# Kernel tuning notes

Measured on AMD Instinct MI355X. Metric: run time of the kernel, lower is better.

Reference implementation:

```python
import jax, jax.numpy as jnp
import numpy as np

N_NODES = 102400
N_EDGES = 1638400
NUM_GRAPHS = 128
IN_DIM = 128
HID = 128
OUT_DIM = 2
NUM_LAYERS = 3
BN_EPS = 1e-5


def setup_inputs() -> dict:
    key = jax.random.key(0)
    ks = jax.random.split(key, 12)
    x = jax.random.normal(ks[0], (N_NODES, IN_DIM), dtype=jnp.float32)
    edge_index = jax.random.randint(ks[1], (2, N_EDGES), 0, N_NODES, dtype=jnp.int64)
    # 128 graphs of 800 nodes each, sorted segment ids
    batch = jnp.repeat(jnp.arange(NUM_GRAPHS, dtype=jnp.int64), N_NODES // NUM_GRAPHS)
    s = 1.0 / np.sqrt(HID)
    W_conv = jax.random.uniform(ks[2], (NUM_LAYERS, HID, HID), jnp.float32, -s, s)
    b_conv = jnp.zeros((NUM_LAYERS, HID), jnp.float32)
    gamma = jnp.ones((NUM_LAYERS, HID), jnp.float32)
    beta = jnp.zeros((NUM_LAYERS, HID), jnp.float32)
    s2 = 1.0 / np.sqrt(3 * HID)
    W_mp1 = jax.random.uniform(ks[3], (3 * HID, 3 * HID), jnp.float32, -s2, s2)
    b_mp1 = jax.random.uniform(ks[4], (3 * HID,), jnp.float32, -s2, s2)
    W_mp2 = jax.random.uniform(ks[5], (3 * HID, OUT_DIM), jnp.float32, -s2, s2)
    b_mp2 = jax.random.uniform(ks[6], (OUT_DIM,), jnp.float32, -s2, s2)
    return {"x": x, "edge_index": edge_index, "batch": batch,
            "W_conv": W_conv, "b_conv": b_conv, "gamma": gamma, "beta": beta,
            "W_mp1": W_mp1, "b_mp1": b_mp1, "W_mp2": W_mp2, "b_mp2": b_mp2}


def _gcn_norm(edge_index, n):
    # add self loops, symmetric normalization: norm_e = deg^-1/2[src] * deg^-1/2[dst]
    loop = jnp.arange(n, dtype=edge_index.dtype)
    src = jnp.concatenate([edge_index[0], loop])
    dst = jnp.concatenate([edge_index[1], loop])
    deg = jax.ops.segment_sum(jnp.ones_like(dst, dtype=jnp.float32), dst, num_segments=n)
    dinv = jnp.where(deg > 0, jax.lax.rsqrt(deg), 0.0)
    return src, dst, dinv[src] * dinv[dst]


def reference(x, edge_index, batch, W_conv, b_conv, gamma, beta, W_mp1, b_mp1, W_mp2, b_mp2):
    n = x.shape[0]
    src, dst, norm = _gcn_norm(edge_index, n)
    for i in range(NUM_LAYERS):
        h = x @ W_conv[i]                                    # [N, HID]
        h = jax.ops.segment_sum(h[src] * norm[:, None], dst, num_segments=n) + b_conv[i]
        h = jax.nn.relu(h)
        mu = jnp.mean(h, axis=0)
        var = jnp.var(h, axis=0)                             # biased, as torch BN
        x = (h - mu) * jax.lax.rsqrt(var + BN_EPS) * gamma[i] + beta[i]
        # dropout p=0.0 -> no-op
    # readout: max pool, mean pool, first-node gather
    x1 = jax.ops.segment_max(x, batch, num_segments=NUM_GRAPHS)
    cnt = jax.ops.segment_sum(jnp.ones((n,), jnp.float32), batch, num_segments=NUM_GRAPHS)
    x2 = jax.ops.segment_sum(x, batch, num_segments=NUM_GRAPHS) / cnt[:, None]
    first_idx = jnp.searchsorted(batch, jnp.arange(NUM_GRAPHS, dtype=batch.dtype))
    x3 = x[first_idx]
    g = jnp.concatenate([x1, x2, x3], axis=1)                # [B, 3*HID]
    g = (g @ W_mp1 + b_mp1) @ W_mp2 + b_mp2
    return jax.nn.log_softmax(g, axis=1)
```

## Files before the change

kernel.cpp:

```cpp
#include <hip/hip_runtime.h>
#include <hip/hip_bf16.h>
#include <cstdint>

#define N_NODESC  102400
#define N_EDGESC  1638400
#define NUM_GRAPHS 128
#define NPG       800
#define HID       128
#define BN_EPS    1e-5f

#define NFINE 1600
#define NCOARSE 25
#define ROUND 2048

typedef short short8 __attribute__((ext_vector_type(8)));
typedef float f32x4  __attribute__((ext_vector_type(4)));
typedef unsigned long long u64;

__device__ __forceinline__ unsigned short f2bf(float f){
    union { __hip_bfloat16 h; unsigned short u; } cv;
    cv.h = __float2bfloat16(f);
    return cv.u;
}
__device__ __forceinline__ float bflo(unsigned int g){ return __uint_as_float(g << 16); }
__device__ __forceinline__ float bfhi(unsigned int g){ return __uint_as_float(g & 0xffff0000u); }
__device__ __forceinline__ float bfu(unsigned short u){ return __uint_as_float(((unsigned int)u) << 16); }

__global__ __launch_bounds__(256) void k_h1(const int* __restrict__ ei, int* __restrict__ fineCount){
    __shared__ int h[NFINE];
    int t = threadIdx.x;
    for (int i = t; i < NFINE; i += 256) h[i] = 0;
    __syncthreads();
    for (int e = blockIdx.x*256 + t; e < N_EDGESC; e += gridDim.x*256){
        int d = __builtin_nontemporal_load(&ei[N_EDGESC + e]);
        atomicAdd(&h[d >> 6], 1);
    }
    __syncthreads();
    for (int i = t; i < NFINE; i += 256) if (h[i]) atomicAdd(&fineCount[i], h[i]);
}

__global__ __launch_bounds__(256) void k_scanF(const int* __restrict__ fineCount, int* __restrict__ fineBase,
                                               int* __restrict__ fineCursor, int* __restrict__ coarseCursor){
    __shared__ int part[256];
    __shared__ int shb[NFINE];
    int t = threadIdx.x;
    int loc[7]; int s = 0;
    #pragma unroll
    for (int j = 0; j < 7; j++){
        int idx = t*7 + j;
        int v = (idx < NFINE) ? fineCount[idx] : 0;
        loc[j] = s; s += v;
    }
    part[t] = s;
    __syncthreads();
    if (t == 0){
        int run = 0;
        for (int i = 0; i < 256; i++){ int v = part[i]; part[i] = run; run += v; }
    }
    __syncthreads();
    #pragma unroll
    for (int j = 0; j < 7; j++){
        int idx = t*7 + j;
        if (idx < NFINE){
            int b = part[t] + loc[j];
            shb[idx] = b;
            fineBase[idx]   = b;
            fineCursor[idx] = b;
        }
    }
    __syncthreads();
    if (t < NCOARSE) coarseCursor[t] = shb[t*64];
}

__global__ __launch_bounds__(256) void k_binA(const int* __restrict__ ei, int* __restrict__ coarseCursor,
                                              u64* __restrict__ coarseBuf){
    __shared__ int cnt[NCOARSE], gpos[NCOARSE], baseS[NCOARSE+1];
    __shared__ u64 stage[ROUND];
    __shared__ short bkt[ROUND];
    int t = threadIdx.x;
    int chunk = blockIdx.x * ROUND;
    if (t < NCOARSE) cnt[t] = 0;
    __syncthreads();
    u64 ed[8]; int b[8], rk[8];
    #pragma unroll
    for (int j = 0; j < 8; j++){
        int e = chunk + t + j*256;
        unsigned int s = (unsigned int)__builtin_nontemporal_load(&ei[e]);
        unsigned int d = (unsigned int)__builtin_nontemporal_load(&ei[N_EDGESC + e]);
        ed[j] = ((u64)d << 32) | (u64)s;
        b[j] = (int)(d >> 12);
        rk[j] = atomicAdd(&cnt[b[j]], 1);
    }
    __syncthreads();
    if (t == 0){
        int s = 0;
        for (int i = 0; i < NCOARSE; i++){ baseS[i] = s; s += cnt[i]; }
        baseS[NCOARSE] = s;
    }
    __syncthreads();
    if (t < NCOARSE && cnt[t] > 0) gpos[t] = atomicAdd(&coarseCursor[t], cnt[t]);
    __syncthreads();
    #pragma unroll
    for (int j = 0; j < 8; j++){
        int p = baseS[b[j]] + rk[j];
        stage[p] = ed[j];
        bkt[p] = (short)b[j];
    }
    __syncthreads();
    #pragma unroll
    for (int j = 0; j < 8; j++){
        int p = t + j*256;
        int bb = bkt[p];
        coarseBuf[gpos[bb] + (p - baseS[bb])] = stage[p];
    }
}

__global__ __launch_bounds__(256) void k_binB(const u64* __restrict__ coarseBuf, const int* __restrict__ fineBase,
                                              int* __restrict__ fineCursor, u64* __restrict__ fineBuf){
    int c   = blockIdx.x >> 5;
    int sub = blockIdx.x & 31;
    int segB = fineBase[c*64];
    int segE = (c == NCOARSE-1) ? N_EDGESC : fineBase[(c+1)*64];
    __shared__ int cnt[64], gpos[64], baseS[65];
    __shared__ u64 stage[ROUND];
    __shared__ short bkt[ROUND];
    int t = threadIdx.x;
    for (int r = sub; ; r += 32){
        int base = segB + r*ROUND;
        if (base >= segE) break;
        int m = segE - base; if (m > ROUND) m = ROUND;
        if (t < 64) cnt[t] = 0;
        __syncthreads();
        u64 ed[8]; int b[8], rk[8], val[8];
        #pragma unroll
        for (int j = 0; j < 8; j++){
            int i = t + j*256;
            val[j] = (i < m);
            if (val[j]){
                ed[j] = __builtin_nontemporal_load(&coarseBuf[base + i]);
                b[j] = (int)((ed[j] >> 38) & 63);
                rk[j] = atomicAdd(&cnt[b[j]], 1);
            }
        }
        __syncthreads();
        if (t == 0){
            int s = 0;
            for (int i = 0; i < 64; i++){ baseS[i] = s; s += cnt[i]; }
            baseS[64] = s;
        }
        __syncthreads();
        if (t < 64 && cnt[t] > 0) gpos[t] = atomicAdd(&fineCursor[c*64 + t], cnt[t]);
        __syncthreads();
        #pragma unroll
        for (int j = 0; j < 8; j++){
            if (val[j]){
                int p = baseS[b[j]] + rk[j];
                stage[p] = ed[j];
                bkt[p] = (short)b[j];
            }
        }
        __syncthreads();
        int total = baseS[64];
        #pragma unroll
        for (int j = 0; j < 8; j++){
            int p = t + j*256;
            if (p < total){
                int bb = bkt[p];
                fineBuf[gpos[bb] + (p - baseS[bb])] = stage[p];
            }
        }
        __syncthreads();
    }
}

__global__ __launch_bounds__(256) void k_binC(const u64* __restrict__ fineBuf, const int* __restrict__ fineBase,
                                              const int* __restrict__ fineCount, int* __restrict__ row_ptr,
                                              float* __restrict__ dinv, int* __restrict__ srcS){
    int f = blockIdx.x, t = threadIdx.x;
    int gB = fineBase[f];
    int cntE = fineCount[f];
    __shared__ int deg[64], excl[64], cur[64];
    if (t < 64){ deg[t] = 0; cur[t] = 0; }
    __syncthreads();
    for (int i = t; i < cntE; i += 256){
        int lo = (int)((fineBuf[gB + i] >> 32) & 63);
        atomicAdd(&deg[lo], 1);
    }
    __syncthreads();
    if (t == 0){
        int s = 0;
        for (int i = 0; i < 64; i++){ excl[i] = s; s += deg[i]; }
    }
    __syncthreads();
    if (t < 64){
        row_ptr[f*64 + t] = gB + excl[t];
        dinv[f*64 + t] = rsqrtf((float)(deg[t] + 1));
    }
    if (f == 0 && t == 0) row_ptr[N_NODESC] = N_EDGESC;
    for (int i = t; i < cntE; i += 256){
        u64 ed = fineBuf[gB + i];
        int lo = (int)((ed >> 32) & 63);
        int pos = gB + excl[lo] + atomicAdd(&cur[lo], 1);
        srcS[pos] = (int)(unsigned int)(ed & 0xffffffffu);
    }
}

__global__ __launch_bounds__(256) void k_prepw0(const float* __restrict__ W, unsigned short* __restrict__ Wt){
    int idx = blockIdx.x*256 + threadIdx.x;
    int n = idx & 127, k = idx >> 7;
    Wt[n*128 + k] = f2bf(W[k*128 + n]);
}

template<int F32IN>
__global__ __launch_bounds__(256) void k_gemm_mfma(const void* __restrict__ Xin,
        const unsigned short* __restrict__ Wt, const float* __restrict__ biasv,
        const float* __restrict__ dinv, unsigned short* __restrict__ H){
    int l   = threadIdx.x & 63;
    int wid = threadIdx.x >> 6;
    int R   = blockIdx.x*64 + wid*16;
    int r0  = l & 15;
    int kg  = l >> 4;
    short8 a[4];
    if (F32IN){
        const float* X = (const float*)Xin;
        #pragma unroll
        for (int kk = 0; kk < 4; kk++){
            const float* p = X + (size_t)(R + r0)*HID + kk*32 + kg*8;
            float4 u = *(const float4*)p;
            float4 v = *(const float4*)(p + 4);
            short8 tt;
            tt[0]=(short)f2bf(u.x); tt[1]=(short)f2bf(u.y); tt[2]=(short)f2bf(u.z); tt[3]=(short)f2bf(u.w);
            tt[4]=(short)f2bf(v.x); tt[5]=(short)f2bf(v.y); tt[6]=(short)f2bf(v.z); tt[7]=(short)f2bf(v.w);
            a[kk] = tt;
        }
    } else {
        const unsigned short* X = (const unsigned short*)Xin;
        #pragma unroll
        for (int kk = 0; kk < 4; kk++)
            a[kk] = *(const short8*)(X + (size_t)(R + r0)*HID + kk*32 + kg*8);
    }
    f32x4 acc[8];
    #pragma unroll
    for (int i = 0; i < 8; i++) acc[i] = (f32x4)(0.f);
    #pragma unroll
    for (int kk = 0; kk < 4; kk++){
        #pragma unroll
        for (int nf = 0; nf < 8; nf++){
            short8 b = *(const short8*)(Wt + (size_t)(nf*16 + r0)*HID + kk*32 + kg*8);
            acc[nf] = __builtin_amdgcn_mfma_f32_16x16x32_bf16(a[kk], b, acc[nf], 0, 0, 0);
        }
    }
    float bv[8];
    #pragma unroll
    for (int nf = 0; nf < 8; nf++) bv[nf] = biasv[nf*16 + r0];
    #pragma unroll
    for (int r = 0; r < 4; r++){
        int row = R + kg*4 + r;
        float di = dinv[row];
        #pragma unroll
        for (int nf = 0; nf < 8; nf++)
            H[(size_t)row*HID + nf*16 + r0] = f2bf(di * (acc[nf][r] + bv[nf]));
    }
}

__global__ __launch_bounds__(256) void k_agg(const unsigned int* __restrict__ Hb, const int* __restrict__ row_ptr,
                                             const int* __restrict__ srcS, const float* __restrict__ dinv,
                                             const float* __restrict__ bconv,
                                             unsigned int* __restrict__ OUT, float* __restrict__ sum,
                                             float* __restrict__ sumsq){
    int lane = threadIdx.x & 63;
    int w    = threadIdx.x >> 6;
    int wave = blockIdx.x*4 + w;
    int nw   = gridDim.x*4;
    float2 bc = ((const float2*)bconv)[lane];
    float sx0 = 0.f, sx1 = 0.f, sq0 = 0.f, sq1 = 0.f;
    for (int n = wave; n < N_NODESC; n += nw){
        int e0 = row_ptr[n], e1 = row_ptr[n+1];
        unsigned int gn = Hb[(size_t)n*64 + lane];
        float ax = bflo(gn), ay = bfhi(gn);
        int e = e0;
        while (e < e1 && (e & 3)){
            unsigned int g = Hb[(size_t)srcS[e]*64 + lane];
            ax += bflo(g); ay += bfhi(g);
            e++;
        }
        for (; e + 8 <= e1; e += 8){
            int4 sa = *(const int4*)(srcS + e);
            int4 sb = *(const int4*)(srcS + e + 4);
            unsigned int g0 = Hb[(size_t)sa.x*64 + lane];
            unsigned int g1 = Hb[(size_t)sa.y*64 + lane];
            unsigned int g2 = Hb[(size_t)sa.z*64 + lane];
            unsigned int g3 = Hb[(size_t)sa.w*64 + lane];
            unsigned int g4 = Hb[(size_t)sb.x*64 + lane];
            unsigned int g5 = Hb[(size_t)sb.y*64 + lane];
            unsigned int g6 = Hb[(size_t)sb.z*64 + lane];
            unsigned int g7 = Hb[(size_t)sb.w*64 + lane];
            ax += bflo(g0); ay += bfhi(g0);
            ax += bflo(g1); ay += bfhi(g1);
            ax += bflo(g2); ay += bfhi(g2);
            ax += bflo(g3); ay += bfhi(g3);
            ax += bflo(g4); ay += bfhi(g4);
            ax += bflo(g5); ay += bfhi(g5);
            ax += bflo(g6); ay += bfhi(g6);
            ax += bflo(g7); ay += bfhi(g7);
        }
        if (e + 4 <= e1){
            int4 sa = *(const int4*)(srcS + e);
            unsigned int g0 = Hb[(size_t)sa.x*64 + lane];
            unsigned int g1 = Hb[(size_t)sa.y*64 + lane];
            unsigned int g2 = Hb[(size_t)sa.z*64 + lane];
            unsigned int g3 = Hb[(size_t)sa.w*64 + lane];
            ax += bflo(g0); ay += bfhi(g0);
            ax += bflo(g1); ay += bfhi(g1);
            ax += bflo(g2); ay += bfhi(g2);
            ax += bflo(g3); ay += bfhi(g3);
            e += 4;
        }
        for (; e < e1; e++){
            unsigned int g = Hb[(size_t)srcS[e]*64 + lane];
            ax += bflo(g); ay += bfhi(g);
        }
        float dn = dinv[n];
        ax = fmaxf(fmaf(ax, dn, bc.x), 0.f);
        ay = fmaxf(fmaf(ay, dn, bc.y), 0.f);
        unsigned int o = ((unsigned int)f2bf(ay) << 16) | (unsigned int)f2bf(ax);
        __builtin_nontemporal_store(o, &OUT[(size_t)n*64 + lane]);
        sx0 += ax; sq0 = fmaf(ax, ax, sq0);
        sx1 += ay; sq1 = fmaf(ay, ay, sq1);
    }
    __shared__ float shs[4][128];
    __shared__ float shq[4][128];
    shs[w][2*lane]   = sx0; shs[w][2*lane+1] = sx1;
    shq[w][2*lane]   = sq0; shq[w][2*lane+1] = sq1;
    __syncthreads();
    int t = threadIdx.x;
    if (t < 128){
        atomicAdd(&sum[t],   shs[0][t] + shs[1][t] + shs[2][t] + shs[3][t]);
        atomicAdd(&sumsq[t], shq[0][t] + shq[1][t] + shq[2][t] + shq[3][t]);
    }
}

__global__ __launch_bounds__(128) void k_fin1(const float* __restrict__ sum, const float* __restrict__ sumsq,
                                              const float* __restrict__ gamma, const float* __restrict__ beta,
                                              const float* __restrict__ Wnext, float* __restrict__ A,
                                              float* __restrict__ B, float* __restrict__ biasv, int hasNext){
    __shared__ float Bsh[128];
    int c = threadIdx.x;
    const float invN = 1.0f / (float)N_NODESC;
    float mu  = sum[c] * invN;
    float var = sumsq[c] * invN - mu*mu;
    float is  = rsqrtf(var + BN_EPS);
    float a = is * gamma[c];
    float b = beta[c] - mu * a;
    A[c] = a; B[c] = b; Bsh[c] = b;
    __syncthreads();
    if (hasNext){
        float bv = 0.f;
        for (int k = 0; k < 128; k++)
            bv = fmaf(Bsh[k], Wnext[k*128 + c], bv);
        biasv[c] = bv;
    }
}

__global__ __launch_bounds__(256) void k_fin2(const float* __restrict__ A, const float* __restrict__ Wnext,
                                              unsigned short* __restrict__ WpT){
    int idx = blockIdx.x*256 + threadIdx.x;
    int c = idx >> 7, k = idx & 127;
    WpT[c*128 + k] = f2bf(A[k] * Wnext[k*128 + c]);
}

__global__ __launch_bounds__(1024) void k_pool(const unsigned short* __restrict__ X, const float* __restrict__ A,
                                               const float* __restrict__ B, float* __restrict__ g){
    __shared__ float shm[8][128];
    __shared__ float shs[8][128];
    int t = threadIdx.x;
    int c = t & 127, sl = t >> 7;
    int gr = blockIdx.x;
    float a = A[c], b = B[c];
    const unsigned short* base = X + ((size_t)gr*NPG + sl*100)*HID;
    float mx = -1e30f, sm = 0.f;
    for (int i = 0; i < 100; i++){
        float v = fmaf(bfu(base[(size_t)i*HID + c]), a, b);
        mx = fmaxf(mx, v); sm += v;
    }
    shm[sl][c] = mx; shs[sl][c] = sm;
    if (sl == 0) g[gr*384 + 256 + c] = fmaf(bfu(base[c]), a, b);
    __syncthreads();
    if (t < 128){
        float m = shm[0][t], s = shs[0][t];
        #pragma unroll
        for (int q = 1; q < 8; q++){ m = fmaxf(m, shm[q][t]); s += shs[q][t]; }
        g[gr*384 + t]       = m;
        g[gr*384 + 128 + t] = s * (1.0f/(float)NPG);
    }
}

__global__ __launch_bounds__(512) void k_mlp(const float* __restrict__ g, const float* __restrict__ W1,
                                             const float* __restrict__ b1, const float* __restrict__ W2,
                                             const float* __restrict__ b2, float* __restrict__ out){
    __shared__ float row[384];
    __shared__ float t1[384];
    __shared__ float r0[512], r1[512];
    int t = threadIdx.x, gr = blockIdx.x;
    if (t < 384) row[t] = g[gr*384 + t];
    __syncthreads();
    if (t < 384){
        float acc = b1[t];
        for (int k = 0; k < 384; k++) acc = fmaf(row[k], W1[(size_t)k*384 + t], acc);
        t1[t] = acc;
    }
    __syncthreads();
    float p0 = 0.f, p1 = 0.f;
    if (t < 384){ float v = t1[t]; p0 = v*W2[t*2]; p1 = v*W2[t*2+1]; }
    r0[t] = p0; r1[t] = p1; __syncthreads();
    for (int off = 256; off > 0; off >>= 1){
        if (t < off){ r0[t] += r0[t+off]; r1[t] += r1[t+off]; }
        __syncthreads();
    }
    if (t == 0){
        float o0 = r0[0] + b2[0], o1 = r1[0] + b2[1];
        float m = fmaxf(o0, o1);
        float lse = m + logf(expf(o0 - m) + expf(o1 - m));
        out[gr*2 + 0] = o0 - lse;
        out[gr*2 + 1] = o1 - lse;
    }
}

extern "C" void kernel_launch(void* const* d_in, const int* in_sizes, int n_in,
                              void* d_out, int out_size, void* d_ws, size_t ws_size,
                              hipStream_t stream){
    const float* x     = (const float*)d_in[0];
    const int*   ei    = (const int*)d_in[1];
    const float* Wconv = (const float*)d_in[3];
    const float* bconv = (const float*)d_in[4];
    const float* gamma = (const float*)d_in[5];
    const float* beta  = (const float*)d_in[6];
    const float* W1    = (const float*)d_in[7];
    const float* b1    = (const float*)d_in[8];
    const float* W2    = (const float*)d_in[9];
    const float* b2    = (const float*)d_in[10];
    float* out = (float*)d_out;

    char* p = (char*)d_ws;
    size_t off = 0;
    auto alloc = [&](size_t bytes)->char* {
        char* r = p + off; off += (bytes + 255) & ~(size_t)255; return r;
    };
    unsigned short* buf1 = (unsigned short*)alloc((size_t)N_NODESC*HID*2);
    unsigned short* buf2 = (unsigned short*)alloc((size_t)N_NODESC*HID*2);
    u64*  coarseBuf  = (u64*)  alloc((size_t)N_EDGESC*8);
    u64*  fineBuf    = (u64*)  alloc((size_t)N_EDGESC*8);
    int*   srcS      = (int*)  alloc((size_t)N_EDGESC*4);
    int*   row_ptr   = (int*)  alloc((size_t)(N_NODESC+1)*4);
    float* dinv      = (float*)alloc((size_t)N_NODESC*4);
    int*   fineCount = (int*)  alloc(NFINE*4);
    int*   fineBase  = (int*)  alloc(NFINE*4);
    int*   fineCursor= (int*)  alloc(NFINE*4);
    int*   coarseCursor=(int*) alloc(NCOARSE*4);
    float* stats   = (float*)alloc(3*2*128*4);
    float* AB      = (float*)alloc(3*2*128*4);
    unsigned short* Wt0 = (unsigned short*)alloc(128*128*2);
    unsigned short* WpT = (unsigned short*)alloc(128*128*2);
    float* biasv   = (float*)alloc(512);
    float* g       = (float*)alloc((size_t)NUM_GRAPHS*384*4);
    (void)ws_size; (void)in_sizes; (void)n_in; (void)out_size;

    hipMemsetAsync(fineCount, 0, NFINE*4, stream);
    hipMemsetAsync(stats, 0, 3*2*128*4, stream);
    hipMemsetAsync(biasv, 0, 512, stream);

    k_h1   <<<256, 256, 0, stream>>>(ei, fineCount);
    k_scanF<<<1,   256, 0, stream>>>(fineCount, fineBase, fineCursor, coarseCursor);
    k_binA <<<N_EDGESC/ROUND, 256, 0, stream>>>(ei, coarseCursor, coarseBuf);
    k_binB <<<NCOARSE*32, 256, 0, stream>>>(coarseBuf, fineBase, fineCursor, fineBuf);
    k_binC <<<NFINE, 256, 0, stream>>>(fineBuf, fineBase, fineCount, row_ptr, dinv, srcS);
    k_prepw0<<<64, 256, 0, stream>>>(Wconv, Wt0);

    for (int l = 0; l < 3; l++){
        if (l == 0)
            k_gemm_mfma<1><<<N_NODESC/64, 256, 0, stream>>>((const void*)x, Wt0, biasv, dinv, buf1);
        else
            k_gemm_mfma<0><<<N_NODESC/64, 256, 0, stream>>>((const void*)buf2, WpT, biasv, dinv, buf1);
        k_agg<<<2048, 256, 0, stream>>>((const unsigned int*)buf1, row_ptr, srcS, dinv,
                                        bconv + l*HID, (unsigned int*)buf2,
                                        stats + l*256, stats + l*256 + 128);
        k_fin1<<<1, 128, 0, stream>>>(stats + l*256, stats + l*256 + 128,
                                      gamma + l*HID, beta + l*HID,
                                      Wconv + (size_t)(l+1 < 3 ? l+1 : 0)*HID*HID,
                                      AB + l*256, AB + l*256 + 128,
                                      biasv, (l < 2) ? 1 : 0);
        if (l < 2)
            k_fin2<<<64, 256, 0, stream>>>(AB + l*256,
                                           Wconv + (size_t)(l+1)*HID*HID, WpT);
    }
    k_pool<<<NUM_GRAPHS, 1024, 0, stream>>>(buf2, AB + 2*256, AB + 2*256 + 128, g);
    k_mlp <<<NUM_GRAPHS, 512, 0, stream>>>(g, W1, b1, W2, b2, out);
}
```

Measured before the change: 546.2 us.

## Interleave two nodes per wave in aggregation and fuse pooling with MLP

The aggregation kernel now has each wave process a pair of adjacent nodes, interleaving their neighbor gathers so more independent loads are in flight per iteration. The old 8-wide unrolled loop is dropped in favour of paired 4-wide loops. Separately, the pool and MLP kernels are fused into one 512-thread kernel, which removes the intermediate buffer and one launch. The biasv memset is folded into the weight-prep kernel. The main risk is load imbalance within a pair, plus higher register use in the aggregation kernel.

```diff
diff --git a/kernel.cpp b/kernel.cpp
--- a/kernel.cpp
+++ b/kernel.cpp
@@ -205,10 +205,12 @@
     }
 }
 
-__global__ __launch_bounds__(256) void k_prepw0(const float* __restrict__ W, unsigned short* __restrict__ Wt){
+__global__ __launch_bounds__(256) void k_prepw0(const float* __restrict__ W, unsigned short* __restrict__ Wt,
+                                                float* __restrict__ biasv){
     int idx = blockIdx.x*256 + threadIdx.x;
     int n = idx & 127, k = idx >> 7;
     Wt[n*128 + k] = f2bf(W[k*128 + n]);
+    if (idx < 128) biasv[idx] = 0.f;
 }
 
 template<int F32IN>
@@ -274,59 +276,77 @@
     int nw   = gridDim.x*4;
     float2 bc = ((const float2*)bconv)[lane];
     float sx0 = 0.f, sx1 = 0.f, sq0 = 0.f, sq1 = 0.f;
-    for (int n = wave; n < N_NODESC; n += nw){
-        int e0 = row_ptr[n], e1 = row_ptr[n+1];
-        unsigned int gn = Hb[(size_t)n*64 + lane];
-        float ax = bflo(gn), ay = bfhi(gn);
-        int e = e0;
-        while (e < e1 && (e & 3)){
-            unsigned int g = Hb[(size_t)srcS[e]*64 + lane];
-            ax += bflo(g); ay += bfhi(g);
-            e++;
-        }
-        for (; e + 8 <= e1; e += 8){
-            int4 sa = *(const int4*)(srcS + e);
-            int4 sb = *(const int4*)(srcS + e + 4);
+    const int NPAIR = N_NODESC/2;
+    for (int pb = wave; pb < NPAIR; pb += nw){
+        int nA = 2*pb, nB = 2*pb + 1;
+        int eA  = row_ptr[nA], e1A = row_ptr[nA+1], e1B = row_ptr[nB+1];
+        int eB  = e1A;
+        unsigned int gsA = Hb[(size_t)nA*64 + lane];
+        unsigned int gsB = Hb[(size_t)nB*64 + lane];
+        float axA = bflo(gsA), ayA = bfhi(gsA);
+        float axB = bflo(gsB), ayB = bfhi(gsB);
+        while (eA + 4 <= e1A && eB + 4 <= e1B){
+            int4 sa = *(const int4*)(srcS + eA);
+            int4 sb = *(const int4*)(srcS + eB);
             unsigned int g0 = Hb[(size_t)sa.x*64 + lane];
             unsigned int g1 = Hb[(size_t)sa.y*64 + lane];
             unsigned int g2 = Hb[(size_t)sa.z*64 + lane];
             unsigned int g3 = Hb[(size_t)sa.w*64 + lane];
-            unsigned int g4 = Hb[(size_t)sb.x*64 + lane];
-            unsigned int g5 = Hb[(size_t)sb.y*64 + lane];
-            unsigned int g6 = Hb[(size_t)sb.z*64 + lane];
-            unsigned int g7 = Hb[(size_t)sb.w*64 + lane];
-            ax += bflo(g0); ay += bfhi(g0);
-            ax += bflo(g1); ay += bfhi(g1);
-            ax += bflo(g2); ay += bfhi(g2);
-            ax += bflo(g3); ay += bfhi(g3);
-            ax += bflo(g4); ay += bfhi(g4);
-            ax += bflo(g5); ay += bfhi(g5);
-            ax += bflo(g6); ay += bfhi(g6);
-            ax += bflo(g7); ay += bfhi(g7);
-        }
-        if (e + 4 <= e1){
-            int4 sa = *(const int4*)(srcS + e);
+            unsigned int h0 = Hb[(size_t)sb.x*64 + lane];
+            unsigned int h1 = Hb[(size_t)sb.y*64 + lane];
+            unsigned int h2 = Hb[(size_t)sb.z*64 + lane];
+            unsigned int h3 = Hb[(size_t)sb.w*64 + lane];
+            axA += bflo(g0); ayA += bfhi(g0);
+            axA += bflo(g1); ayA += bfhi(g1);
+            axA += bflo(g2); ayA += bfhi(g2);
+            axA += bflo(g3); ayA += bfhi(g3);
+            axB += bflo(h0); ayB += bfhi(h0);
+            axB += bflo(h1); ayB += bfhi(h1);
+            axB += bflo(h2); ayB += bfhi(h2);
+            axB += bflo(h3); ayB += bfhi(h3);
+            eA += 4; eB += 4;
+        }
+        for (; eA + 4 <= e1A; eA += 4){
+            int4 sa = *(const int4*)(srcS + eA);
             unsigned int g0 = Hb[(size_t)sa.x*64 + lane];
             unsigned int g1 = Hb[(size_t)sa.y*64 + lane];
             unsigned int g2 = Hb[(size_t)sa.z*64 + lane];
             unsigned int g3 = Hb[(size_t)sa.w*64 + lane];
-            ax += bflo(g0); ay += bfhi(g0);
-            ax += bflo(g1); ay += bfhi(g1);
-            ax += bflo(g2); ay += bfhi(g2);
-            ax += bflo(g3); ay += bfhi(g3);
-            e += 4;
-        }
-        for (; e < e1; e++){
-            unsigned int g = Hb[(size_t)srcS[e]*64 + lane];
-            ax += bflo(g); ay += bfhi(g);
-        }
-        float dn = dinv[n];
-        ax = fmaxf(fmaf(ax, dn, bc.x), 0.f);
-        ay = fmaxf(fmaf(ay, dn, bc.y), 0.f);
-        unsigned int o = ((unsigned int)f2bf(ay) << 16) | (unsigned int)f2bf(ax);
-        __builtin_nontemporal_store(o, &OUT[(size_t)n*64 + lane]);
-        sx0 += ax; sq0 = fmaf(ax, ax, sq0);
-        sx1 += ay; sq1 = fmaf(ay, ay, sq1);
+            axA += bflo(g0); ayA += bfhi(g0);
+            axA += bflo(g1); ayA += bfhi(g1);
+            axA += bflo(g2); ayA += bfhi(g2);
+            axA += bflo(g3); ayA += bfhi(g3);
+        }
+        for (; eB + 4 <= e1B; eB += 4){
+            int4 sb = *(const int4*)(srcS + eB);
+            unsigned int h0 = Hb[(size_t)sb.x*64 + lane];
+            unsigned int h1 = Hb[(size_t)sb.y*64 + lane];
+            unsigned int h2 = Hb[(size_t)sb.z*64 + lane];
+            unsigned int h3 = Hb[(size_t)sb.w*64 + lane];
+            axB += bflo(h0); ayB += bfhi(h0);
+            axB += bflo(h1); ayB += bfhi(h1);
+            axB += bflo(h2); ayB += bfhi(h2);
+            axB += bflo(h3); ayB += bfhi(h3);
+        }
+        while (eA < e1A || eB < e1B){
+            unsigned int g = 0, h = 0;
+            int doA = (eA < e1A), doB = (eB < e1B);
+            if (doA) g = Hb[(size_t)srcS[eA]*64 + lane];
+            if (doB) h = Hb[(size_t)srcS[eB]*64 + lane];
+            if (doA){ axA += bflo(g); ayA += bfhi(g); eA++; }
+            if (doB){ axB += bflo(h); ayB += bfhi(h); eB++; }
+        }
+        float dA = dinv[nA], dB = dinv[nB];
+        axA = fmaxf(fmaf(axA, dA, bc.x), 0.f);
+        ayA = fmaxf(fmaf(ayA, dA, bc.y), 0.f);
+        axB = fmaxf(fmaf(axB, dB, bc.x), 0.f);
+        ayB = fmaxf(fmaf(ayB, dB, bc.y), 0.f);
+        unsigned int oA = ((unsigned int)f2bf(ayA) << 16) | (unsigned int)f2bf(axA);
+        unsigned int oB = ((unsigned int)f2bf(ayB) << 16) | (unsigned int)f2bf(axB);
+        __builtin_nontemporal_store(oA, &OUT[(size_t)nA*64 + lane]);
+        __builtin_nontemporal_store(oB, &OUT[(size_t)nB*64 + lane]);
+        sx0 += axA + axB; sq0 += axA*axA + axB*axB;
+        sx1 += ayA + ayB; sq1 += ayA*ayA + ayB*ayB;
     }
     __shared__ float shs[4][128];
     __shared__ float shq[4][128];
@@ -369,40 +389,33 @@
     WpT[c*128 + k] = f2bf(A[k] * Wnext[k*128 + c]);
 }
 
-__global__ __launch_bounds__(1024) void k_pool(const unsigned short* __restrict__ X, const float* __restrict__ A,
-                                               const float* __restrict__ B, float* __restrict__ g){
-    __shared__ float shm[8][128];
-    __shared__ float shs[8][128];
-    int t = threadIdx.x;
-    int c = t & 127, sl = t >> 7;
-    int gr = blockIdx.x;
-    float a = A[c], b = B[c];
-    const unsigned short* base = X + ((size_t)gr*NPG + sl*100)*HID;
-    float mx = -1e30f, sm = 0.f;
-    for (int i = 0; i < 100; i++){
-        float v = fmaf(bfu(base[(size_t)i*HID + c]), a, b);
-        mx = fmaxf(mx, v); sm += v;
-    }
-    shm[sl][c] = mx; shs[sl][c] = sm;
-    if (sl == 0) g[gr*384 + 256 + c] = fmaf(bfu(base[c]), a, b);
-    __syncthreads();
-    if (t < 128){
-        float m = shm[0][t], s = shs[0][t];
-        #pragma unroll
-        for (int q = 1; q < 8; q++){ m = fmaxf(m, shm[q][t]); s += shs[q][t]; }
-        g[gr*384 + t]       = m;
-        g[gr*384 + 128 + t] = s * (1.0f/(float)NPG);
-    }
-}
-
-__global__ __launch_bounds__(512) void k_mlp(const float* __restrict__ g, const float* __restrict__ W1,
-                                             const float* __restrict__ b1, const float* __restrict__ W2,
-                                             const float* __restrict__ b2, float* __restrict__ out){
+__global__ __launch_bounds__(512) void k_poolmlp(const unsigned short* __restrict__ X, const float* __restrict__ A,
+                                                 const float* __restrict__ B, const float* __restrict__ W1,
+                                                 const float* __restrict__ b1, const float* __restrict__ W2,
+                                                 const float* __restrict__ b2, float* __restrict__ out){
+    __shared__ float shm[4][128];
+    __shared__ float shsm[4][128];
     __shared__ float row[384];
     __shared__ float t1[384];
     __shared__ float r0[512], r1[512];
     int t = threadIdx.x, gr = blockIdx.x;
-    if (t < 384) row[t] = g[gr*384 + t];
+    int c = t & 127, sl = t >> 7;
+    float a = A[c], b = B[c];
+    const unsigned short* base = X + ((size_t)gr*NPG + sl*200)*HID;
+    float mx = -1e30f, sm = 0.f;
+    for (int i = 0; i < 200; i++){
+        float v = fmaf(bfu(base[(size_t)i*HID + c]), a, b);
+        mx = fmaxf(mx, v); sm += v;
+    }
+    shm[sl][c] = mx; shsm[sl][c] = sm;
+    if (sl == 0) row[256 + c] = fmaf(bfu(base[c]), a, b);
+    __syncthreads();
+    if (t < 128){
+        float m = fmaxf(fmaxf(shm[0][t], shm[1][t]), fmaxf(shm[2][t], shm[3][t]));
+        float s = shsm[0][t] + shsm[1][t] + shsm[2][t] + shsm[3][t];
+        row[t]       = m;
+        row[128 + t] = s * (1.0f/(float)NPG);
+    }
     __syncthreads();
     if (t < 384){
         float acc = b1[t];
@@ -462,19 +475,17 @@
     unsigned short* Wt0 = (unsigned short*)alloc(128*128*2);
     unsigned short* WpT = (unsigned short*)alloc(128*128*2);
     float* biasv   = (float*)alloc(512);
-    float* g       = (float*)alloc((size_t)NUM_GRAPHS*384*4);
     (void)ws_size; (void)in_sizes; (void)n_in; (void)out_size;
 
     hipMemsetAsync(fineCount, 0, NFINE*4, stream);
     hipMemsetAsync(stats, 0, 3*2*128*4, stream);
-    hipMemsetAsync(biasv, 0, 512, stream);
 
     k_h1   <<<256, 256, 0, stream>>>(ei, fineCount);
     k_scanF<<<1,   256, 0, stream>>>(fineCount, fineBase, fineCursor, coarseCursor);
     k_binA <<<N_EDGESC/ROUND, 256, 0, stream>>>(ei, coarseCursor, coarseBuf);
     k_binB <<<NCOARSE*32, 256, 0, stream>>>(coarseBuf, fineBase, fineCursor, fineBuf);
     k_binC <<<NFINE, 256, 0, stream>>>(fineBuf, fineBase, fineCount, row_ptr, dinv, srcS);
-    k_prepw0<<<64, 256, 0, stream>>>(Wconv, Wt0);
+    k_prepw0<<<64, 256, 0, stream>>>(Wconv, Wt0, biasv);
 
     for (int l = 0; l < 3; l++){
         if (l == 0)
@@ -493,6 +504,6 @@
             k_fin2<<<64, 256, 0, stream>>>(AB + l*256,
                                            Wconv + (size_t)(l+1)*HID*HID, WpT);
     }
-    k_pool<<<NUM_GRAPHS, 1024, 0, stream>>>(buf2, AB + 2*256, AB + 2*256 + 128, g);
-    k_mlp <<<NUM_GRAPHS, 512, 0, stream>>>(g, W1, b1, W2, b2, out);
-}
+    k_poolmlp<<<NUM_GRAPHS, 512, 0, stream>>>(buf2, AB + 2*256, AB + 2*256 + 128,
+                                              W1, b1, W2, b2, out);
+}
```

Measured after the change: 531.1 us. 2.8% less time.
